# Optimization experiments

Measured on AMD Instinct MI355X. Metric: run time of the kernel, lower is better.

The kernel has to match this reference:

```python
import jax, jax.numpy as jnp
import numpy as np

D = 256  # subgraph_width
N_CLASSES = 10
EPS = 1e-5  # torch LayerNorm default


def _layernorm(x, g, b):
    mu = jnp.mean(x, axis=-1, keepdims=True)
    var = jnp.var(x, axis=-1, keepdims=True)
    return (x - mu) * jax.lax.rsqrt(var + EPS) * g + b


def setup_inputs() -> dict:
    key = jax.random.key(0)
    ks = jax.random.split(key, 16)
    B, T, N = 64, 512, 512
    traj = jax.random.normal(ks[0], (B, T, 2), dtype=jnp.float32)
    labels = jax.random.randint(ks[1], (B,), 0, N_CLASSES)
    h = jax.random.normal(ks[2], (B, N, D), dtype=jnp.float32)
    valid_len = jnp.maximum(jax.random.randint(ks[3], (B,), 0, N), 1)
    s = 0.02
    params = dict(
        emb=jax.random.normal(ks[4], (N_CLASSES, D), dtype=jnp.float32) * s,
        w_mlp=jax.random.normal(ks[5], (2, D), dtype=jnp.float32) * s,
        b_mlp=jnp.zeros((D,), jnp.float32),
        ln_g=jnp.ones((D,), jnp.float32),
        ln_b=jnp.zeros((D,), jnp.float32),
        wq=jax.random.normal(ks[6], (D, D), dtype=jnp.float32) * s,
        bq=jnp.zeros((D,), jnp.float32),
        wk=jax.random.normal(ks[7], (D, D), dtype=jnp.float32) * s,
        bk=jnp.zeros((D,), jnp.float32),
        wv=jax.random.normal(ks[8], (D, D), dtype=jnp.float32) * s,
        bv=jnp.zeros((D,), jnp.float32),
        w_out=jax.random.normal(ks[9], (D, 1), dtype=jnp.float32) * s,
        b_out=jnp.zeros((1,), jnp.float32),
    )
    return dict(traj=traj, labels=labels, h=h, valid_len=valid_len, **params)


def reference(traj, labels, h, valid_len, emb, w_mlp, b_mlp, ln_g, ln_b,
              wq, bq, wk, bk, wv, bv, w_out, b_out):
    # MLP(in=2, out=D, activation='leaky'): Linear -> LayerNorm -> LeakyReLU
    x = jax.nn.leaky_relu(_layernorm(traj @ w_mlp + b_mlp, ln_g, ln_b))  # [B,T,D]
    le = emb[labels]                          # [B,D]
    x = x + le[:, None, :]                    # embed-add
    # SelfAttentionWithKeyFCLayer: Q from x, K/V from h, scaled, key-masked by valid_len
    q = x @ wq + bq                            # [B,T,D]
    k = h @ wk + bk                            # [B,N,D]
    v = h @ wv + bv                            # [B,N,D]
    scores = jnp.einsum('btd,bnd->btn', q, k) / jnp.sqrt(jnp.float32(D))
    N = h.shape[1]
    key_mask = jnp.arange(N)[None, :] < valid_len[:, None]          # [B,N]
    scores = jnp.where(key_mask[:, None, :], scores, jnp.float32(-1e9))
    attn = jax.nn.softmax(scores, axis=-1)
    enc = jnp.einsum('btn,bnd->btd', attn, v)  # [B,T,D]
    pooled = jnp.max(enc, axis=1) + le          # [B,D]
    return jax.nn.sigmoid(pooled @ w_out + b_out)  # [B,1]
```

## Files before the change

### kernel.cpp

```cpp
#include <hip/hip_runtime.h>
#include <math.h>

typedef float f32x4 __attribute__((ext_vector_type(4)));
typedef __bf16 bf16x8 __attribute__((ext_vector_type(8)));
typedef unsigned short u16x8 __attribute__((ext_vector_type(8)));
typedef unsigned short u16x4 __attribute__((ext_vector_type(4)));
typedef unsigned int u32x4 __attribute__((ext_vector_type(4)));

#define MFMA(a, b, c) __builtin_amdgcn_mfma_f32_16x16x32_bf16((a), (b), (c), 0, 0, 0)

static __device__ __forceinline__ unsigned short f2bf(float f) {
  unsigned u = __float_as_uint(f);
  u += 0x7FFFu + ((u >> 16) & 1u);
  return (unsigned short)(u >> 16);
}
static __device__ __forceinline__ float bf2f(unsigned short s) {
  return __uint_as_float(((unsigned)s) << 16);
}
static __device__ __forceinline__ unsigned pack2bf(float lo, float hi) {
  return (unsigned)f2bf(lo) | ((unsigned)f2bf(hi) << 16);
}

static __device__ __forceinline__ int swz512(int row, int col) {
  return row * 512 + (col ^ ((((row & 7) ^ (col >> 6)) & 7) << 4));
}
static __device__ __forceinline__ int swzV(int d, int col) {
  return d * 64 + (col ^ (((d >> 1) & 3) << 4));
}
static __device__ __forceinline__ int swzO(int d, int col) {
  return d * 256 + (col ^ ((((d & 7) ^ (col >> 7)) & 7) << 4));
}

__global__ __launch_bounds__(256) void setup(
    const float* __restrict__ w0m, const float* __restrict__ w1m, const float* __restrict__ w2m,
    unsigned short* __restrict__ t0m, unsigned short* __restrict__ t1m, unsigned short* __restrict__ t2m,
    const float* __restrict__ w_mlp, const float* __restrict__ b_mlp, float* __restrict__ lnsc,
    const int* __restrict__ vlen, int* __restrict__ tasktab) {
  int bid = blockIdx.x;
  int t = threadIdx.x;
  if (bid == 48) {
    float w0 = w_mlp[t], w1 = w_mlp[256 + t], bb = b_mlp[t];
    float v[9] = {w0, w1, bb, w0 * w0, w1 * w1, w0 * w1, w0 * bb, w1 * bb, bb * bb};
    __shared__ float red[4][9];
#pragma unroll
    for (int j = 0; j < 9; ++j) {
      float s = v[j];
#pragma unroll
      for (int off = 32; off >= 1; off >>= 1) s += __shfl_xor(s, off, 64);
      v[j] = s;
    }
    if ((t & 63) == 0)
      for (int j = 0; j < 9; ++j) red[t >> 6][j] = v[j];
    __syncthreads();
    if (t < 9) lnsc[t] = red[0][t] + red[1][t] + red[2][t] + red[3][t];
    return;
  }
  if (bid == 49) {
    __shared__ int srank[64];
    if (t < 64) {
      int vb = vlen[t], r = 0;
      for (int j = 0; j < 64; ++j) {
        int vj = vlen[j];
        r += (vj > vb) || (vj == vb && j < t);
      }
      srank[r] = t;
    }
    __syncthreads();
    if (t < 64) {
      int r = t, b = srank[r];
      int xcd = r & 7, a = r >> 3;
      for (int tt = 0; tt < 4; ++tt)
        tasktab[(a * 4 + tt) * 8 + xcd] = (b << 2) | tt;
    }
    return;
  }
  int m = bid >> 4, t16 = bid & 15;
  const float* w = (m == 0) ? w0m : (m == 1) ? w1m : w2m;
  unsigned short* o = (m == 0) ? t0m : (m == 1) ? t1m : t2m;
  __shared__ float sm[64][65];
  int bi = t16 >> 2, bj = t16 & 3;
  for (int kb = 0; kb < 16; ++kb) {
    int idx = kb * 256 + t;
    int r = idx >> 6, c = idx & 63;
    sm[r][c] = w[(bi * 64 + r) * 256 + bj * 64 + c];
  }
  __syncthreads();
  for (int kb = 0; kb < 16; ++kb) {
    int idx = kb * 256 + t;
    int r = idx >> 6, c = idx & 63;
    int d = bj * 64 + r, e = bi * 64 + c;
    o[(e >> 5) * 8192 + d * 32 + (e & 31)] = f2bf(sm[c][r]);
  }
}

static __device__ __forceinline__ void gemm_direct(
    const unsigned short* __restrict__ Bpk, const unsigned short* Alds,
    int w, int g, int c15, f32x4 (&acc)[4][4]) {
  const unsigned short* bp = Bpk + (w * 64 + c15) * 32 + 8 * g;
#pragma unroll
  for (int c = 0; c < 8; ++c) {
    bf16x8 bfv[4];
#pragma unroll
    for (int nt = 0; nt < 4; ++nt)
      bfv[nt] = *(const bf16x8*)(bp + c * 8192 + nt * 512);
    bf16x8 af[4];
#pragma unroll
    for (int at = 0; at < 4; ++at)
      af[at] = *(const bf16x8*)((char*)Alds + swz512(at * 16 + c15, c * 64 + 16 * g));
    __builtin_amdgcn_s_setprio(1);
#pragma unroll
    for (int at = 0; at < 4; ++at)
#pragma unroll
      for (int nt = 0; nt < 4; ++nt) acc[at][nt] = MFMA(af[at], bfv[nt], acc[at][nt]);
    __builtin_amdgcn_s_setprio(0);
  }
}

__global__ __launch_bounds__(256, 4) void gemms(
    const float* __restrict__ traj, const int* __restrict__ labels, const float* __restrict__ emb,
    const float* __restrict__ w_mlp, const float* __restrict__ b_mlp,
    const float* __restrict__ ln_g, const float* __restrict__ ln_b,
    const float* __restrict__ lnsc, const unsigned short* __restrict__ wqPk,
    const float* __restrict__ bq, unsigned short* __restrict__ q,
    const float* __restrict__ h, const int* __restrict__ vlen,
    const unsigned short* __restrict__ wkPk, const float* __restrict__ bk,
    const unsigned short* __restrict__ wvPk, const float* __restrict__ bv,
    unsigned short* __restrict__ kout, unsigned short* __restrict__ vT) {
  __shared__ unsigned short Alds[64 * 256];
  int tid = threadIdx.x, w = tid >> 6, lane = tid & 63, g = lane >> 4, c15 = lane & 15;
  int bid = blockIdx.x;
  f32x4 acc[4][4];

  if (bid < 512) {
    int tile = bid, b = tile >> 3;
    {
      int rrow = tid >> 5, cb = (tid & 31) * 8;
      int lab = labels[b];
      f32x4 wa0 = *(const f32x4*)(w_mlp + cb), wa1 = *(const f32x4*)(w_mlp + cb + 4);
      f32x4 wb0 = *(const f32x4*)(w_mlp + 256 + cb), wb1 = *(const f32x4*)(w_mlp + 256 + cb + 4);
      f32x4 bm0 = *(const f32x4*)(b_mlp + cb), bm1 = *(const f32x4*)(b_mlp + cb + 4);
      f32x4 g0 = *(const f32x4*)(ln_g + cb), g1 = *(const f32x4*)(ln_g + cb + 4);
      f32x4 lb0 = *(const f32x4*)(ln_b + cb), lb1 = *(const f32x4*)(ln_b + cb + 4);
      f32x4 le0 = *(const f32x4*)(emb + lab * 256 + cb), le1 = *(const f32x4*)(emb + lab * 256 + cb + 4);
      float s0 = lnsc[0], s1 = lnsc[1], s2 = lnsc[2], s3 = lnsc[3], s4 = lnsc[4],
            s5 = lnsc[5], s6 = lnsc[6], s7 = lnsc[7], s8 = lnsc[8];
#pragma unroll
      for (int i = 0; i < 8; ++i) {
        int row = i * 8 + rrow, grow = tile * 64 + row;
        float t0 = traj[grow * 2], t1 = traj[grow * 2 + 1];
        float mu = (t0 * s0 + t1 * s1 + s2) * (1.f / 256.f);
        float ea2 = (t0 * t0 * s3 + t1 * t1 * s4 + s8 +
                     2.f * (t0 * t1 * s5 + t0 * s6 + t1 * s7)) * (1.f / 256.f);
        float rstd = rsqrtf(ea2 - mu * mu + 1e-5f);
        u16x8 pk;
#pragma unroll
        for (int j = 0; j < 4; ++j) {
          float a0 = t0 * wa0[j] + t1 * wb0[j] + bm0[j];
          float y0 = (a0 - mu) * rstd * g0[j] + lb0[j];
          pk[j] = f2bf((y0 > 0.f ? y0 : 0.01f * y0) + le0[j]);
          float a1 = t0 * wa1[j] + t1 * wb1[j] + bm1[j];
          float y1 = (a1 - mu) * rstd * g1[j] + lb1[j];
          pk[j + 4] = f2bf((y1 > 0.f ? y1 : 0.01f * y1) + le1[j]);
        }
        *(u16x8*)((char*)Alds + swz512(row, cb * 2)) = pk;
      }
    }
#pragma unroll
    for (int a = 0; a < 4; ++a)
#pragma unroll
      for (int n = 0; n < 4; ++n) acc[a][n] = (f32x4){0.f, 0.f, 0.f, 0.f};
    __syncthreads();
    gemm_direct(wqPk, Alds, w, g, c15, acc);
    __syncthreads();
#pragma unroll
    for (int at = 0; at < 4; ++at)
#pragma unroll
      for (int nt = 0; nt < 4; ++nt) {
        int col = w * 64 + nt * 16 + c15;
        float bb = bq[col];
#pragma unroll
        for (int r = 0; r < 4; ++r)
          *(unsigned short*)((char*)Alds + swz512(at * 16 + 4 * g + r, col * 2)) =
              f2bf(acc[at][nt][r] + bb);
      }
    __syncthreads();
    {
      int row = tid >> 2;
      for (int i = 0; i < 8; ++i) {
        int colb = (tid & 3) * 128 + i * 16;
        u16x8 vv = *(const u16x8*)((char*)Alds + swz512(row, colb));
        *(u16x8*)(q + (size_t)(tile * 64 + row) * 256 + colb / 2) = vv;
      }
    }
    return;
  }

  int tile = bid - 512;
  int b = tile >> 3;
  int nbase = (tile & 7) * 64;
  if (nbase >= vlen[b]) return;
  {
    const float* hb = h + (size_t)tile * 16384;
    f32x4 ha[8], hc[8];
#pragma unroll
    for (int i = 0; i < 8; ++i) {
      ha[i] = *(const f32x4*)(hb + i * 2048 + tid * 8);
      hc[i] = *(const f32x4*)(hb + i * 2048 + tid * 8 + 4);
    }
#pragma unroll
    for (int i = 0; i < 8; ++i) {
      u16x8 pk;
#pragma unroll
      for (int j = 0; j < 4; ++j) { pk[j] = f2bf(ha[i][j]); pk[j + 4] = f2bf(hc[i][j]); }
      *(u16x8*)((char*)Alds + swz512(i * 8 + (tid >> 5), (tid & 31) * 16)) = pk;
    }
  }
#pragma unroll
  for (int a = 0; a < 4; ++a)
#pragma unroll
    for (int n = 0; n < 4; ++n) acc[a][n] = (f32x4){0.f, 0.f, 0.f, 0.f};
  __syncthreads();

  gemm_direct(wvPk, Alds, w, g, c15, acc);
#pragma unroll
  for (int at = 0; at < 4; ++at)
#pragma unroll
    for (int nt = 0; nt < 4; ++nt) {
      int col = w * 64 + nt * 16 + c15;
      float bb = bv[col];
      u16x4 o;
#pragma unroll
      for (int r = 0; r < 4; ++r) o[r] = f2bf(acc[at][nt][r] + bb);
      *(u16x4*)(vT + (size_t)b * 131072 + (size_t)col * 512 + nbase + at * 16 + 4 * g) = o;
    }

#pragma unroll
  for (int a = 0; a < 4; ++a)
#pragma unroll
    for (int n = 0; n < 4; ++n) acc[a][n] = (f32x4){0.f, 0.f, 0.f, 0.f};
  gemm_direct(wkPk, Alds, w, g, c15, acc);
  __syncthreads();
#pragma unroll
  for (int at = 0; at < 4; ++at)
#pragma unroll
    for (int nt = 0; nt < 4; ++nt) {
      int col = w * 64 + nt * 16 + c15;
      float bb = bk[col];
#pragma unroll
      for (int r = 0; r < 4; ++r)
        *(unsigned short*)((char*)Alds + swz512(at * 16 + 4 * g + r, col * 2)) =
            f2bf(acc[at][nt][r] + bb);
    }
  __syncthreads();
  {
    int row = tid >> 2;
    for (int i = 0; i < 8; ++i) {
      int colb = (tid & 3) * 128 + i * 16;
      u16x8 vv = *(const u16x8*)((char*)Alds + swz512(row, colb));
      *(u16x8*)(kout + (size_t)(tile * 64 + row) * 256 + colb / 2) = vv;
    }
  }
}

__global__ __launch_bounds__(512) void attn(
    const unsigned short* __restrict__ q, const unsigned short* __restrict__ k,
    const unsigned short* __restrict__ vT, const int* __restrict__ valid_len,
    const int* __restrict__ tasktab, float* __restrict__ partial) {
  __shared__ unsigned short buf[2][16384];

  int task = tasktab[blockIdx.x];
  int b = task >> 2, tt = task & 3;
  int tid = threadIdx.x, w = tid >> 6, lane = tid & 63, g = lane >> 4, c15 = lane & 15;
  int vl = valid_len[b];
  int nit = (vl + 31) >> 5;

  bf16x8 qf[8];
  size_t qrow = (size_t)b * 512 + tt * 128 + w * 16 + c15;
#pragma unroll
  for (int kk = 0; kk < 8; ++kk)
    qf[kk] = *(const bf16x8*)(q + qrow * 256 + kk * 32 + 8 * g);

  f32x4 acco[16];
#pragma unroll
  for (int i = 0; i < 16; ++i) acco[i] = (f32x4){0.f, 0.f, 0.f, 0.f};
  float rs = 0.f;

  const unsigned short* kbase = k + (size_t)b * 512 * 256;
  const unsigned short* vbase = vT + (size_t)b * 131072;
  u16x8 kpre[2], vpre[2];

#pragma unroll
  for (int i = 0; i < 2; ++i) {
    int idx = tid + 512 * i, key = idx >> 5, s = idx & 31;
    kpre[i] = *(const u16x8*)(kbase + (size_t)key * 256 + s * 8);
  }
#pragma unroll
  for (int i = 0; i < 2; ++i) {
    int idx = tid + 512 * i, d = idx >> 2, s = idx & 3;
    vpre[i] = *(const u16x8*)(vbase + (size_t)d * 512 + s * 8);
  }
#pragma unroll
  for (int i = 0; i < 2; ++i) {
    int idx = tid + 512 * i, key = idx >> 5, s = idx & 31;
    *(u16x8*)((char*)buf[0] + swz512(key, s * 16)) = kpre[i];
  }
#pragma unroll
  for (int i = 0; i < 2; ++i) {
    int idx = tid + 512 * i, d = idx >> 2, s = idx & 3;
    *(u16x8*)((char*)(buf[0] + 8192) + swzV(d, s * 16)) = vpre[i];
  }

  for (int it = 0; it < nit; ++it) {
    int cur = it & 1;
    __syncthreads();
    bool pf = (it + 1 < nit);
    if (pf) {
      int n1 = (it + 1) * 32;
#pragma unroll
      for (int i = 0; i < 2; ++i) {
        int idx = tid + 512 * i, key = idx >> 5, s = idx & 31;
        kpre[i] = *(const u16x8*)(kbase + (size_t)(n1 + key) * 256 + s * 8);
      }
#pragma unroll
      for (int i = 0; i < 2; ++i) {
        int idx = tid + 512 * i, d = idx >> 2, s = idx & 3;
        vpre[i] = *(const u16x8*)(vbase + (size_t)d * 512 + n1 + s * 8);
      }
    }
    unsigned short* Klds = buf[cur];
    unsigned short* Vlds = buf[cur] + 8192;
    int n0 = it * 32;

    float p[2][4];
    unsigned u01[2], u23[2];
#pragma unroll
    for (int c = 0; c < 2; ++c) {
      f32x4 s4 = (f32x4){0.f, 0.f, 0.f, 0.f};
      __builtin_amdgcn_s_setprio(1);
#pragma unroll
      for (int kk = 0; kk < 8; ++kk) {
        bf16x8 kf = *(const bf16x8*)((char*)Klds + swz512(c * 16 + c15, kk * 64 + 16 * g));
        s4 = MFMA(kf, qf[kk], s4);
      }
      __builtin_amdgcn_s_setprio(0);
#pragma unroll
      for (int r = 0; r < 4; ++r) {
        int key = n0 + c * 16 + 4 * g + r;
        float pv = (key < vl) ? __expf(s4[r] * 0.0625f) : 0.f;
        p[c][r] = pv;
        rs += pv;
      }
      u01[c] = pack2bf(p[c][0], p[c][1]);
      u23[c] = pack2bf(p[c][2], p[c][3]);
    }
    int srcA = c15 | ((lane & 16) << 1);
    int srcB = srcA + 16;
    unsigned x0a = (unsigned)__shfl((int)u01[0], srcA, 64);
    unsigned x1a = (unsigned)__shfl((int)u01[1], srcA, 64);
    unsigned x0b = (unsigned)__shfl((int)u23[0], srcA, 64);
    unsigned x1b = (unsigned)__shfl((int)u23[1], srcA, 64);
    unsigned x0c = (unsigned)__shfl((int)u01[0], srcB, 64);
    unsigned x1c = (unsigned)__shfl((int)u01[1], srcB, 64);
    unsigned x0d = (unsigned)__shfl((int)u23[0], srcB, 64);
    unsigned x1d = (unsigned)__shfl((int)u23[1], srcB, 64);
    bool hi = g >= 2;
    union { u32x4 u; bf16x8 v; } pa;
    pa.u[0] = hi ? x1a : x0a;
    pa.u[1] = hi ? x1b : x0b;
    pa.u[2] = hi ? x1c : x0c;
    pa.u[3] = hi ? x1d : x0d;
    __builtin_amdgcn_s_setprio(1);
#pragma unroll
    for (int dt = 0; dt < 16; ++dt) {
      bf16x8 vf = *(const bf16x8*)((char*)Vlds + swzV(dt * 16 + c15, 16 * g));
      acco[dt] = MFMA(vf, pa.v, acco[dt]);
    }
    __builtin_amdgcn_s_setprio(0);
    if (pf) {
      unsigned short* Kn = buf[cur ^ 1];
      unsigned short* Vn = buf[cur ^ 1] + 8192;
#pragma unroll
      for (int i = 0; i < 2; ++i) {
        int idx = tid + 512 * i, key = idx >> 5, s = idx & 31;
        *(u16x8*)((char*)Kn + swz512(key, s * 16)) = kpre[i];
      }
#pragma unroll
      for (int i = 0; i < 2; ++i) {
        int idx = tid + 512 * i, d = idx >> 2, s = idx & 3;
        *(u16x8*)((char*)Vn + swzV(d, s * 16)) = vpre[i];
      }
    }
  }
  rs += __shfl_xor(rs, 16, 64);
  rs += __shfl_xor(rs, 32, 64);
  float inv = 1.f / rs;
  __syncthreads();
  int qcol = w * 16 + c15;
#pragma unroll
  for (int dt = 0; dt < 16; ++dt)
#pragma unroll
    for (int r = 0; r < 4; ++r) {
      int d = dt * 16 + 4 * g + r;
      *(unsigned short*)((char*)buf + swzO(d, qcol * 2)) = f2bf(acco[dt][r] * inv);
    }
  __syncthreads();
  {
    int d = tid & 255, half = tid >> 8;
    float m = -1e30f;
    for (int i = 0; i < 8; ++i) {
      u16x8 vv = *(const u16x8*)((char*)buf + swzO(d, half * 128 + i * 16));
#pragma unroll
      for (int j = 0; j < 8; ++j) m = fmaxf(m, bf2f(vv[j]));
    }
    partial[(((size_t)b * 4 + tt) * 2 + half) * 256 + d] = m;
  }
}

__global__ __launch_bounds__(256) void finalize(
    const float* __restrict__ partial, const float* __restrict__ emb,
    const int* __restrict__ labels, const float* __restrict__ w_out,
    const float* __restrict__ b_out, float* __restrict__ out) {
  int b = blockIdx.x, t = threadIdx.x;
  float m = -1e30f;
#pragma unroll
  for (int s8 = 0; s8 < 8; ++s8)
    m = fmaxf(m, partial[((size_t)b * 8 + s8) * 256 + t]);
  m += emb[labels[b] * 256 + t];
  __shared__ float red[256];
  red[t] = m * w_out[t];
  __syncthreads();
  for (int s = 128; s > 0; s >>= 1) {
    if (t < s) red[t] += red[t + s];
    __syncthreads();
  }
  if (t == 0) out[b] = 1.f / (1.f + __expf(-(red[0] + b_out[0])));
}

extern "C" void kernel_launch(void* const* d_in, const int* in_sizes, int n_in,
                              void* d_out, int out_size, void* d_ws, size_t ws_size,
                              hipStream_t stream) {
  const float* traj   = (const float*)d_in[0];
  const int*   labels = (const int*)d_in[1];
  const float* h      = (const float*)d_in[2];
  const int*   vlen   = (const int*)d_in[3];
  const float* emb    = (const float*)d_in[4];
  const float* w_mlp  = (const float*)d_in[5];
  const float* b_mlp  = (const float*)d_in[6];
  const float* ln_g   = (const float*)d_in[7];
  const float* ln_b   = (const float*)d_in[8];
  const float* wq     = (const float*)d_in[9];
  const float* bq     = (const float*)d_in[10];
  const float* wk     = (const float*)d_in[11];
  const float* bk     = (const float*)d_in[12];
  const float* wv     = (const float*)d_in[13];
  const float* bv     = (const float*)d_in[14];
  const float* w_out  = (const float*)d_in[15];
  const float* b_out  = (const float*)d_in[16];
  float* out = (float*)d_out;

  unsigned short* qb   = (unsigned short*)d_ws;
  unsigned short* kb   = qb + (size_t)32768 * 256;
  unsigned short* vT   = kb + (size_t)32768 * 256;
  unsigned short* wqPk = vT + (size_t)32768 * 256;
  unsigned short* wkPk = wqPk + 65536;
  unsigned short* wvPk = wkPk + 65536;
  float* lnsc    = (float*)(wvPk + 65536);
  float* partial = lnsc + 16;
  int*   tasktab = (int*)(partial + 64 * 8 * 256);

  setup<<<50, 256, 0, stream>>>(wq, wk, wv, wqPk, wkPk, wvPk, w_mlp, b_mlp, lnsc,
                                vlen, tasktab);
  gemms<<<1024, 256, 0, stream>>>(traj, labels, emb, w_mlp, b_mlp, ln_g, ln_b,
                                  lnsc, wqPk, bq, qb, h, vlen, wkPk, bk, wvPk, bv,
                                  kb, vT);
  attn<<<256, 512, 0, stream>>>(qb, kb, vT, vlen, tasktab, partial);
  finalize<<<64, 256, 0, stream>>>(partial, emb, labels, w_out, b_out, out);
}
```

Before: 76.83 us.

## Fuse MLP/LayerNorm and Q projection into attention kernel, 2 query tiles per wave

The embedding MLP, LayerNorm and Q GEMM move out of the gemms kernel and into the attention kernel. Each attention block computes its 128 query rows in LDS and keeps them in registers, so the bf16 Q round trip through global memory goes away and the gemms launch shrinks to the K/V blocks only. The attention block drops from 512 to 256 threads, and each wave now handles two 16-row query tiles. Each K/V fragment loaded from LDS is therefore reused for twice as many MFMAs. The trade-off is much higher register pressure (launch_bounds 1) and fewer waves per block for latency hiding, with the Q GEMM now serialized ahead of the attention loop.

```diff
diff --git a/kernel.cpp b/kernel.cpp
--- a/kernel.cpp
+++ b/kernel.cpp
@@ -117,88 +117,17 @@
 }
 
 __global__ __launch_bounds__(256, 4) void gemms(
-    const float* __restrict__ traj, const int* __restrict__ labels, const float* __restrict__ emb,
-    const float* __restrict__ w_mlp, const float* __restrict__ b_mlp,
-    const float* __restrict__ ln_g, const float* __restrict__ ln_b,
-    const float* __restrict__ lnsc, const unsigned short* __restrict__ wqPk,
-    const float* __restrict__ bq, unsigned short* __restrict__ q,
     const float* __restrict__ h, const int* __restrict__ vlen,
     const unsigned short* __restrict__ wkPk, const float* __restrict__ bk,
     const unsigned short* __restrict__ wvPk, const float* __restrict__ bv,
     unsigned short* __restrict__ kout, unsigned short* __restrict__ vT) {
   __shared__ unsigned short Alds[64 * 256];
   int tid = threadIdx.x, w = tid >> 6, lane = tid & 63, g = lane >> 4, c15 = lane & 15;
-  int bid = blockIdx.x;
-  f32x4 acc[4][4];
-
-  if (bid < 512) {
-    int tile = bid, b = tile >> 3;
-    {
-      int rrow = tid >> 5, cb = (tid & 31) * 8;
-      int lab = labels[b];
-      f32x4 wa0 = *(const f32x4*)(w_mlp + cb), wa1 = *(const f32x4*)(w_mlp + cb + 4);
-      f32x4 wb0 = *(const f32x4*)(w_mlp + 256 + cb), wb1 = *(const f32x4*)(w_mlp + 256 + cb + 4);
-      f32x4 bm0 = *(const f32x4*)(b_mlp + cb), bm1 = *(const f32x4*)(b_mlp + cb + 4);
-      f32x4 g0 = *(const f32x4*)(ln_g + cb), g1 = *(const f32x4*)(ln_g + cb + 4);
-      f32x4 lb0 = *(const f32x4*)(ln_b + cb), lb1 = *(const f32x4*)(ln_b + cb + 4);
-      f32x4 le0 = *(const f32x4*)(emb + lab * 256 + cb), le1 = *(const f32x4*)(emb + lab * 256 + cb + 4);
-      float s0 = lnsc[0], s1 = lnsc[1], s2 = lnsc[2], s3 = lnsc[3], s4 = lnsc[4],
-            s5 = lnsc[5], s6 = lnsc[6], s7 = lnsc[7], s8 = lnsc[8];
-#pragma unroll
-      for (int i = 0; i < 8; ++i) {
-        int row = i * 8 + rrow, grow = tile * 64 + row;
-        float t0 = traj[grow * 2], t1 = traj[grow * 2 + 1];
-        float mu = (t0 * s0 + t1 * s1 + s2) * (1.f / 256.f);
-        float ea2 = (t0 * t0 * s3 + t1 * t1 * s4 + s8 +
-                     2.f * (t0 * t1 * s5 + t0 * s6 + t1 * s7)) * (1.f / 256.f);
-        float rstd = rsqrtf(ea2 - mu * mu + 1e-5f);
-        u16x8 pk;
-#pragma unroll
-        for (int j = 0; j < 4; ++j) {
-          float a0 = t0 * wa0[j] + t1 * wb0[j] + bm0[j];
-          float y0 = (a0 - mu) * rstd * g0[j] + lb0[j];
-          pk[j] = f2bf((y0 > 0.f ? y0 : 0.01f * y0) + le0[j]);
-          float a1 = t0 * wa1[j] + t1 * wb1[j] + bm1[j];
-          float y1 = (a1 - mu) * rstd * g1[j] + lb1[j];
-          pk[j + 4] = f2bf((y1 > 0.f ? y1 : 0.01f * y1) + le1[j]);
-        }
-        *(u16x8*)((char*)Alds + swz512(row, cb * 2)) = pk;
-      }
-    }
-#pragma unroll
-    for (int a = 0; a < 4; ++a)
-#pragma unroll
-      for (int n = 0; n < 4; ++n) acc[a][n] = (f32x4){0.f, 0.f, 0.f, 0.f};
-    __syncthreads();
-    gemm_direct(wqPk, Alds, w, g, c15, acc);
-    __syncthreads();
-#pragma unroll
-    for (int at = 0; at < 4; ++at)
-#pragma unroll
-      for (int nt = 0; nt < 4; ++nt) {
-        int col = w * 64 + nt * 16 + c15;
-        float bb = bq[col];
-#pragma unroll
-        for (int r = 0; r < 4; ++r)
-          *(unsigned short*)((char*)Alds + swz512(at * 16 + 4 * g + r, col * 2)) =
-              f2bf(acc[at][nt][r] + bb);
-      }
-    __syncthreads();
-    {
-      int row = tid >> 2;
-      for (int i = 0; i < 8; ++i) {
-        int colb = (tid & 3) * 128 + i * 16;
-        u16x8 vv = *(const u16x8*)((char*)Alds + swz512(row, colb));
-        *(u16x8*)(q + (size_t)(tile * 64 + row) * 256 + colb / 2) = vv;
-      }
-    }
-    return;
-  }
-
-  int tile = bid - 512;
+  int tile = blockIdx.x;
   int b = tile >> 3;
   int nbase = (tile & 7) * 64;
   if (nbase >= vlen[b]) return;
+  f32x4 acc[4][4];
   {
     const float* hb = h + (size_t)tile * 16384;
     f32x4 ha[8], hc[8];
@@ -262,10 +191,15 @@
   }
 }
 
-__global__ __launch_bounds__(512) void attn(
-    const unsigned short* __restrict__ q, const unsigned short* __restrict__ k,
-    const unsigned short* __restrict__ vT, const int* __restrict__ valid_len,
-    const int* __restrict__ tasktab, float* __restrict__ partial) {
+__global__ __launch_bounds__(256, 1) void attn(
+    const float* __restrict__ traj, const int* __restrict__ labels,
+    const float* __restrict__ emb, const float* __restrict__ w_mlp,
+    const float* __restrict__ b_mlp, const float* __restrict__ ln_g,
+    const float* __restrict__ ln_b, const float* __restrict__ lnsc,
+    const unsigned short* __restrict__ wqPk, const float* __restrict__ bq,
+    const unsigned short* __restrict__ k, const unsigned short* __restrict__ vT,
+    const int* __restrict__ valid_len, const int* __restrict__ tasktab,
+    float* __restrict__ partial) {
   __shared__ unsigned short buf[2][16384];
 
   int task = tasktab[blockIdx.x];
@@ -274,39 +208,115 @@
   int vl = valid_len[b];
   int nit = (vl + 31) >> 5;
 
-  bf16x8 qf[8];
-  size_t qrow = (size_t)b * 512 + tt * 128 + w * 16 + c15;
-#pragma unroll
-  for (int kk = 0; kk < 8; ++kk)
-    qf[kk] = *(const bf16x8*)(q + qrow * 256 + kk * 32 + 8 * g);
-
-  f32x4 acco[16];
-#pragma unroll
-  for (int i = 0; i < 16; ++i) acco[i] = (f32x4){0.f, 0.f, 0.f, 0.f};
-  float rs = 0.f;
+  {
+    int rrow = tid >> 5, cb = (tid & 31) * 8;
+    int lab = labels[b];
+    f32x4 wa0 = *(const f32x4*)(w_mlp + cb), wa1 = *(const f32x4*)(w_mlp + cb + 4);
+    f32x4 wb0 = *(const f32x4*)(w_mlp + 256 + cb), wb1 = *(const f32x4*)(w_mlp + 256 + cb + 4);
+    f32x4 bm0 = *(const f32x4*)(b_mlp + cb), bm1 = *(const f32x4*)(b_mlp + cb + 4);
+    f32x4 g0 = *(const f32x4*)(ln_g + cb), g1 = *(const f32x4*)(ln_g + cb + 4);
+    f32x4 lb0 = *(const f32x4*)(ln_b + cb), lb1 = *(const f32x4*)(ln_b + cb + 4);
+    f32x4 le0 = *(const f32x4*)(emb + lab * 256 + cb), le1 = *(const f32x4*)(emb + lab * 256 + cb + 4);
+    float s0 = lnsc[0], s1 = lnsc[1], s2 = lnsc[2], s3 = lnsc[3], s4 = lnsc[4],
+          s5 = lnsc[5], s6 = lnsc[6], s7 = lnsc[7], s8 = lnsc[8];
+#pragma unroll
+    for (int i = 0; i < 16; ++i) {
+      int row = i * 8 + rrow, grow = b * 512 + tt * 128 + row;
+      float t0 = traj[grow * 2], t1 = traj[grow * 2 + 1];
+      float mu = (t0 * s0 + t1 * s1 + s2) * (1.f / 256.f);
+      float ea2 = (t0 * t0 * s3 + t1 * t1 * s4 + s8 +
+                   2.f * (t0 * t1 * s5 + t0 * s6 + t1 * s7)) * (1.f / 256.f);
+      float rstd = rsqrtf(ea2 - mu * mu + 1e-5f);
+      u16x8 pk;
+#pragma unroll
+      for (int j = 0; j < 4; ++j) {
+        float a0 = t0 * wa0[j] + t1 * wb0[j] + bm0[j];
+        float y0 = (a0 - mu) * rstd * g0[j] + lb0[j];
+        pk[j] = f2bf((y0 > 0.f ? y0 : 0.01f * y0) + le0[j]);
+        float a1 = t0 * wa1[j] + t1 * wb1[j] + bm1[j];
+        float y1 = (a1 - mu) * rstd * g1[j] + lb1[j];
+        pk[j + 4] = f2bf((y1 > 0.f ? y1 : 0.01f * y1) + le1[j]);
+      }
+      *(u16x8*)((char*)buf + swz512(row, cb * 2)) = pk;
+    }
+  }
+  __syncthreads();
+
+  f32x4 qacc[8][4];
+#pragma unroll
+  for (int a = 0; a < 8; ++a)
+#pragma unroll
+    for (int n = 0; n < 4; ++n) qacc[a][n] = (f32x4){0.f, 0.f, 0.f, 0.f};
+  {
+    const unsigned short* bp = wqPk + (w * 64 + c15) * 32 + 8 * g;
+#pragma unroll
+    for (int c = 0; c < 8; ++c) {
+      bf16x8 bfv[4];
+#pragma unroll
+      for (int nt = 0; nt < 4; ++nt)
+        bfv[nt] = *(const bf16x8*)(bp + c * 8192 + nt * 512);
+      bf16x8 af[8];
+#pragma unroll
+      for (int at = 0; at < 8; ++at)
+        af[at] = *(const bf16x8*)((char*)buf + swz512(at * 16 + c15, c * 64 + 16 * g));
+      __builtin_amdgcn_s_setprio(1);
+#pragma unroll
+      for (int at = 0; at < 8; ++at)
+#pragma unroll
+        for (int nt = 0; nt < 4; ++nt) qacc[at][nt] = MFMA(af[at], bfv[nt], qacc[at][nt]);
+      __builtin_amdgcn_s_setprio(0);
+    }
+  }
+  __syncthreads();
+#pragma unroll
+  for (int nt = 0; nt < 4; ++nt) {
+    int col = w * 64 + nt * 16 + c15;
+    float bb = bq[col];
+#pragma unroll
+    for (int at = 0; at < 8; ++at)
+#pragma unroll
+      for (int r = 0; r < 4; ++r)
+        *(unsigned short*)((char*)buf + swz512(at * 16 + 4 * g + r, col * 2)) =
+            f2bf(qacc[at][nt][r] + bb);
+  }
+  __syncthreads();
+  bf16x8 qf[2][8];
+#pragma unroll
+  for (int qt = 0; qt < 2; ++qt)
+#pragma unroll
+    for (int kk = 0; kk < 8; ++kk)
+      qf[qt][kk] = *(const bf16x8*)((char*)buf + swz512(qt * 64 + w * 16 + c15, kk * 64 + 16 * g));
+  __syncthreads();
+
+  f32x4 acco[2][16];
+#pragma unroll
+  for (int qt = 0; qt < 2; ++qt)
+#pragma unroll
+    for (int i = 0; i < 16; ++i) acco[qt][i] = (f32x4){0.f, 0.f, 0.f, 0.f};
+  float rs[2] = {0.f, 0.f};
 
   const unsigned short* kbase = k + (size_t)b * 512 * 256;
   const unsigned short* vbase = vT + (size_t)b * 131072;
-  u16x8 kpre[2], vpre[2];
-
-#pragma unroll
-  for (int i = 0; i < 2; ++i) {
-    int idx = tid + 512 * i, key = idx >> 5, s = idx & 31;
+  u16x8 kpre[4], vpre[4];
+
+#pragma unroll
+  for (int i = 0; i < 4; ++i) {
+    int idx = tid + 256 * i, key = idx >> 5, s = idx & 31;
     kpre[i] = *(const u16x8*)(kbase + (size_t)key * 256 + s * 8);
   }
 #pragma unroll
-  for (int i = 0; i < 2; ++i) {
-    int idx = tid + 512 * i, d = idx >> 2, s = idx & 3;
+  for (int i = 0; i < 4; ++i) {
+    int idx = tid + 256 * i, d = idx >> 2, s = idx & 3;
     vpre[i] = *(const u16x8*)(vbase + (size_t)d * 512 + s * 8);
   }
 #pragma unroll
-  for (int i = 0; i < 2; ++i) {
-    int idx = tid + 512 * i, key = idx >> 5, s = idx & 31;
+  for (int i = 0; i < 4; ++i) {
+    int idx = tid + 256 * i, key = idx >> 5, s = idx & 31;
     *(u16x8*)((char*)buf[0] + swz512(key, s * 16)) = kpre[i];
   }
 #pragma unroll
-  for (int i = 0; i < 2; ++i) {
-    int idx = tid + 512 * i, d = idx >> 2, s = idx & 3;
+  for (int i = 0; i < 4; ++i) {
+    int idx = tid + 256 * i, d = idx >> 2, s = idx & 3;
     *(u16x8*)((char*)(buf[0] + 8192) + swzV(d, s * 16)) = vpre[i];
   }
 
@@ -317,13 +327,13 @@
     if (pf) {
       int n1 = (it + 1) * 32;
 #pragma unroll
-      for (int i = 0; i < 2; ++i) {
-        int idx = tid + 512 * i, key = idx >> 5, s = idx & 31;
+      for (int i = 0; i < 4; ++i) {
+        int idx = tid + 256 * i, key = idx >> 5, s = idx & 31;
         kpre[i] = *(const u16x8*)(kbase + (size_t)(n1 + key) * 256 + s * 8);
       }
 #pragma unroll
-      for (int i = 0; i < 2; ++i) {
-        int idx = tid + 512 * i, d = idx >> 2, s = idx & 3;
+      for (int i = 0; i < 4; ++i) {
+        int idx = tid + 256 * i, d = idx >> 2, s = idx & 3;
         vpre[i] = *(const u16x8*)(vbase + (size_t)d * 512 + n1 + s * 8);
       }
     }
@@ -331,88 +341,108 @@
     unsigned short* Vlds = buf[cur] + 8192;
     int n0 = it * 32;
 
-    float p[2][4];
-    unsigned u01[2], u23[2];
-#pragma unroll
-    for (int c = 0; c < 2; ++c) {
-      f32x4 s4 = (f32x4){0.f, 0.f, 0.f, 0.f};
-      __builtin_amdgcn_s_setprio(1);
+    f32x4 s4[2][2];
+#pragma unroll
+    for (int qt = 0; qt < 2; ++qt)
+#pragma unroll
+      for (int c = 0; c < 2; ++c) s4[qt][c] = (f32x4){0.f, 0.f, 0.f, 0.f};
+    __builtin_amdgcn_s_setprio(1);
+#pragma unroll
+    for (int c = 0; c < 2; ++c)
 #pragma unroll
       for (int kk = 0; kk < 8; ++kk) {
         bf16x8 kf = *(const bf16x8*)((char*)Klds + swz512(c * 16 + c15, kk * 64 + 16 * g));
-        s4 = MFMA(kf, qf[kk], s4);
-      }
-      __builtin_amdgcn_s_setprio(0);
-#pragma unroll
-      for (int r = 0; r < 4; ++r) {
-        int key = n0 + c * 16 + 4 * g + r;
-        float pv = (key < vl) ? __expf(s4[r] * 0.0625f) : 0.f;
-        p[c][r] = pv;
-        rs += pv;
-      }
-      u01[c] = pack2bf(p[c][0], p[c][1]);
-      u23[c] = pack2bf(p[c][2], p[c][3]);
-    }
+        s4[0][c] = MFMA(kf, qf[0][kk], s4[0][c]);
+        s4[1][c] = MFMA(kf, qf[1][kk], s4[1][c]);
+      }
+    __builtin_amdgcn_s_setprio(0);
+    unsigned u01[2][2], u23[2][2];
+#pragma unroll
+    for (int qt = 0; qt < 2; ++qt)
+#pragma unroll
+      for (int c = 0; c < 2; ++c) {
+        float p4[4];
+#pragma unroll
+        for (int r = 0; r < 4; ++r) {
+          int key = n0 + c * 16 + 4 * g + r;
+          float pv = (key < vl) ? __expf(s4[qt][c][r] * 0.0625f) : 0.f;
+          p4[r] = pv;
+          rs[qt] += pv;
+        }
+        u01[qt][c] = pack2bf(p4[0], p4[1]);
+        u23[qt][c] = pack2bf(p4[2], p4[3]);
+      }
     int srcA = c15 | ((lane & 16) << 1);
     int srcB = srcA + 16;
-    unsigned x0a = (unsigned)__shfl((int)u01[0], srcA, 64);
-    unsigned x1a = (unsigned)__shfl((int)u01[1], srcA, 64);
-    unsigned x0b = (unsigned)__shfl((int)u23[0], srcA, 64);
-    unsigned x1b = (unsigned)__shfl((int)u23[1], srcA, 64);
-    unsigned x0c = (unsigned)__shfl((int)u01[0], srcB, 64);
-    unsigned x1c = (unsigned)__shfl((int)u01[1], srcB, 64);
-    unsigned x0d = (unsigned)__shfl((int)u23[0], srcB, 64);
-    unsigned x1d = (unsigned)__shfl((int)u23[1], srcB, 64);
     bool hi = g >= 2;
-    union { u32x4 u; bf16x8 v; } pa;
-    pa.u[0] = hi ? x1a : x0a;
-    pa.u[1] = hi ? x1b : x0b;
-    pa.u[2] = hi ? x1c : x0c;
-    pa.u[3] = hi ? x1d : x0d;
+    union { u32x4 u; bf16x8 v; } pa[2];
+#pragma unroll
+    for (int qt = 0; qt < 2; ++qt) {
+      unsigned x0a = (unsigned)__shfl((int)u01[qt][0], srcA, 64);
+      unsigned x1a = (unsigned)__shfl((int)u01[qt][1], srcA, 64);
+      unsigned x0b = (unsigned)__shfl((int)u23[qt][0], srcA, 64);
+      unsigned x1b = (unsigned)__shfl((int)u23[qt][1], srcA, 64);
+      unsigned x0c = (unsigned)__shfl((int)u01[qt][0], srcB, 64);
+      unsigned x1c = (unsigned)__shfl((int)u01[qt][1], srcB, 64);
+      unsigned x0d = (unsigned)__shfl((int)u23[qt][0], srcB, 64);
+      unsigned x1d = (unsigned)__shfl((int)u23[qt][1], srcB, 64);
+      pa[qt].u[0] = hi ? x1a : x0a;
+      pa[qt].u[1] = hi ? x1b : x0b;
+      pa[qt].u[2] = hi ? x1c : x0c;
+      pa[qt].u[3] = hi ? x1d : x0d;
+    }
     __builtin_amdgcn_s_setprio(1);
 #pragma unroll
     for (int dt = 0; dt < 16; ++dt) {
       bf16x8 vf = *(const bf16x8*)((char*)Vlds + swzV(dt * 16 + c15, 16 * g));
-      acco[dt] = MFMA(vf, pa.v, acco[dt]);
+      acco[0][dt] = MFMA(vf, pa[0].v, acco[0][dt]);
+      acco[1][dt] = MFMA(vf, pa[1].v, acco[1][dt]);
     }
     __builtin_amdgcn_s_setprio(0);
     if (pf) {
       unsigned short* Kn = buf[cur ^ 1];
       unsigned short* Vn = buf[cur ^ 1] + 8192;
 #pragma unroll
-      for (int i = 0; i < 2; ++i) {
-        int idx = tid + 512 * i, key = idx >> 5, s = idx & 31;
+      for (int i = 0; i < 4; ++i) {
+        int idx = tid + 256 * i, key = idx >> 5, s = idx & 31;
         *(u16x8*)((char*)Kn + swz512(key, s * 16)) = kpre[i];
       }
 #pragma unroll
-      for (int i = 0; i < 2; ++i) {
-        int idx = tid + 512 * i, d = idx >> 2, s = idx & 3;
+      for (int i = 0; i < 4; ++i) {
+        int idx = tid + 256 * i, d = idx >> 2, s = idx & 3;
         *(u16x8*)((char*)Vn + swzV(d, s * 16)) = vpre[i];
       }
     }
   }
-  rs += __shfl_xor(rs, 16, 64);
-  rs += __shfl_xor(rs, 32, 64);
-  float inv = 1.f / rs;
-  __syncthreads();
-  int qcol = w * 16 + c15;
-#pragma unroll
-  for (int dt = 0; dt < 16; ++dt)
-#pragma unroll
-    for (int r = 0; r < 4; ++r) {
-      int d = dt * 16 + 4 * g + r;
-      *(unsigned short*)((char*)buf + swzO(d, qcol * 2)) = f2bf(acco[dt][r] * inv);
-    }
+  float inv[2];
+#pragma unroll
+  for (int qt = 0; qt < 2; ++qt) {
+    rs[qt] += __shfl_xor(rs[qt], 16, 64);
+    rs[qt] += __shfl_xor(rs[qt], 32, 64);
+    inv[qt] = 1.f / rs[qt];
+  }
+  __syncthreads();
+#pragma unroll
+  for (int qt = 0; qt < 2; ++qt) {
+    int qcol = qt * 64 + w * 16 + c15;
+#pragma unroll
+    for (int dt = 0; dt < 16; ++dt)
+#pragma unroll
+      for (int r = 0; r < 4; ++r) {
+        int d = dt * 16 + 4 * g + r;
+        *(unsigned short*)((char*)buf + swzO(d, qcol * 2)) = f2bf(acco[qt][dt][r] * inv[qt]);
+      }
+  }
   __syncthreads();
   {
-    int d = tid & 255, half = tid >> 8;
+    int d = tid;
     float m = -1e30f;
-    for (int i = 0; i < 8; ++i) {
-      u16x8 vv = *(const u16x8*)((char*)buf + swzO(d, half * 128 + i * 16));
+    for (int i = 0; i < 16; ++i) {
+      u16x8 vv = *(const u16x8*)((char*)buf + swzO(d, i * 16));
 #pragma unroll
       for (int j = 0; j < 8; ++j) m = fmaxf(m, bf2f(vv[j]));
     }
-    partial[(((size_t)b * 4 + tt) * 2 + half) * 256 + d] = m;
+    partial[((size_t)b * 4 + tt) * 256 + d] = m;
   }
 }
 
@@ -423,8 +453,8 @@
   int b = blockIdx.x, t = threadIdx.x;
   float m = -1e30f;
 #pragma unroll
-  for (int s8 = 0; s8 < 8; ++s8)
-    m = fmaxf(m, partial[((size_t)b * 8 + s8) * 256 + t]);
+  for (int s4 = 0; s4 < 4; ++s4)
+    m = fmaxf(m, partial[((size_t)b * 4 + s4) * 256 + t]);
   m += emb[labels[b] * 256 + t];
   __shared__ float red[256];
   red[t] = m * w_out[t];
@@ -458,21 +488,19 @@
   const float* b_out  = (const float*)d_in[16];
   float* out = (float*)d_out;
 
-  unsigned short* qb   = (unsigned short*)d_ws;
-  unsigned short* kb   = qb + (size_t)32768 * 256;
+  unsigned short* kb   = (unsigned short*)d_ws;
   unsigned short* vT   = kb + (size_t)32768 * 256;
   unsigned short* wqPk = vT + (size_t)32768 * 256;
   unsigned short* wkPk = wqPk + 65536;
   unsigned short* wvPk = wkPk + 65536;
   float* lnsc    = (float*)(wvPk + 65536);
   float* partial = lnsc + 16;
-  int*   tasktab = (int*)(partial + 64 * 8 * 256);
+  int*   tasktab = (int*)(partial + 64 * 4 * 256);
 
   setup<<<50, 256, 0, stream>>>(wq, wk, wv, wqPk, wkPk, wvPk, w_mlp, b_mlp, lnsc,
                                 vlen, tasktab);
-  gemms<<<1024, 256, 0, stream>>>(traj, labels, emb, w_mlp, b_mlp, ln_g, ln_b,
-                                  lnsc, wqPk, bq, qb, h, vlen, wkPk, bk, wvPk, bv,
-                                  kb, vT);
-  attn<<<256, 512, 0, stream>>>(qb, kb, vT, vlen, tasktab, partial);
+  gemms<<<512, 256, 0, stream>>>(h, vlen, wkPk, bk, wvPk, bv, kb, vT);
+  attn<<<256, 256, 0, stream>>>(traj, labels, emb, w_mlp, b_mlp, ln_g, ln_b, lnsc,
+                                wqPk, bq, kb, vT, vlen, tasktab, partial);
   finalize<<<64, 256, 0, stream>>>(partial, emb, labels, w_out, b_out, out);
 }
```

Measured after the change: 86.46 us. +12.5%, slower.

## Fuse Q projection into attention kernel and split K/V GEMMs across waves

Applied to the files above, without the earlier changes.

The MLP+LayerNorm+embedding prologue and the Q projection move from the gemms kernel into the attention kernel. Each attention block now computes its own 128 rows of Q in LDS and reads them straight into registers, so Q is never written to or read back from global memory. The gemms kernel becomes K/V only, launched with 512-thread blocks where four waves compute V and four compute K concurrently, using a separate LDS buffer for K. The cost is extra prologue work and synchronisation inside the attention kernel, plus higher register and LDS pressure there.

```diff
diff --git a/kernel.cpp b/kernel.cpp
--- a/kernel.cpp
+++ b/kernel.cpp
@@ -116,103 +116,33 @@
   }
 }
 
-__global__ __launch_bounds__(256, 4) void gemms(
-    const float* __restrict__ traj, const int* __restrict__ labels, const float* __restrict__ emb,
-    const float* __restrict__ w_mlp, const float* __restrict__ b_mlp,
-    const float* __restrict__ ln_g, const float* __restrict__ ln_b,
-    const float* __restrict__ lnsc, const unsigned short* __restrict__ wqPk,
-    const float* __restrict__ bq, unsigned short* __restrict__ q,
+__global__ __launch_bounds__(512, 4) void gemms(
     const float* __restrict__ h, const int* __restrict__ vlen,
     const unsigned short* __restrict__ wkPk, const float* __restrict__ bk,
     const unsigned short* __restrict__ wvPk, const float* __restrict__ bv,
     unsigned short* __restrict__ kout, unsigned short* __restrict__ vT) {
   __shared__ unsigned short Alds[64 * 256];
+  __shared__ unsigned short Klds[64 * 256];
   int tid = threadIdx.x, w = tid >> 6, lane = tid & 63, g = lane >> 4, c15 = lane & 15;
-  int bid = blockIdx.x;
-  f32x4 acc[4][4];
-
-  if (bid < 512) {
-    int tile = bid, b = tile >> 3;
-    {
-      int rrow = tid >> 5, cb = (tid & 31) * 8;
-      int lab = labels[b];
-      f32x4 wa0 = *(const f32x4*)(w_mlp + cb), wa1 = *(const f32x4*)(w_mlp + cb + 4);
-      f32x4 wb0 = *(const f32x4*)(w_mlp + 256 + cb), wb1 = *(const f32x4*)(w_mlp + 256 + cb + 4);
-      f32x4 bm0 = *(const f32x4*)(b_mlp + cb), bm1 = *(const f32x4*)(b_mlp + cb + 4);
-      f32x4 g0 = *(const f32x4*)(ln_g + cb), g1 = *(const f32x4*)(ln_g + cb + 4);
-      f32x4 lb0 = *(const f32x4*)(ln_b + cb), lb1 = *(const f32x4*)(ln_b + cb + 4);
-      f32x4 le0 = *(const f32x4*)(emb + lab * 256 + cb), le1 = *(const f32x4*)(emb + lab * 256 + cb + 4);
-      float s0 = lnsc[0], s1 = lnsc[1], s2 = lnsc[2], s3 = lnsc[3], s4 = lnsc[4],
-            s5 = lnsc[5], s6 = lnsc[6], s7 = lnsc[7], s8 = lnsc[8];
-#pragma unroll
-      for (int i = 0; i < 8; ++i) {
-        int row = i * 8 + rrow, grow = tile * 64 + row;
-        float t0 = traj[grow * 2], t1 = traj[grow * 2 + 1];
-        float mu = (t0 * s0 + t1 * s1 + s2) * (1.f / 256.f);
-        float ea2 = (t0 * t0 * s3 + t1 * t1 * s4 + s8 +
-                     2.f * (t0 * t1 * s5 + t0 * s6 + t1 * s7)) * (1.f / 256.f);
-        float rstd = rsqrtf(ea2 - mu * mu + 1e-5f);
-        u16x8 pk;
-#pragma unroll
-        for (int j = 0; j < 4; ++j) {
-          float a0 = t0 * wa0[j] + t1 * wb0[j] + bm0[j];
-          float y0 = (a0 - mu) * rstd * g0[j] + lb0[j];
-          pk[j] = f2bf((y0 > 0.f ? y0 : 0.01f * y0) + le0[j]);
-          float a1 = t0 * wa1[j] + t1 * wb1[j] + bm1[j];
-          float y1 = (a1 - mu) * rstd * g1[j] + lb1[j];
-          pk[j + 4] = f2bf((y1 > 0.f ? y1 : 0.01f * y1) + le1[j]);
-        }
-        *(u16x8*)((char*)Alds + swz512(row, cb * 2)) = pk;
-      }
-    }
-#pragma unroll
-    for (int a = 0; a < 4; ++a)
-#pragma unroll
-      for (int n = 0; n < 4; ++n) acc[a][n] = (f32x4){0.f, 0.f, 0.f, 0.f};
-    __syncthreads();
-    gemm_direct(wqPk, Alds, w, g, c15, acc);
-    __syncthreads();
-#pragma unroll
-    for (int at = 0; at < 4; ++at)
-#pragma unroll
-      for (int nt = 0; nt < 4; ++nt) {
-        int col = w * 64 + nt * 16 + c15;
-        float bb = bq[col];
-#pragma unroll
-        for (int r = 0; r < 4; ++r)
-          *(unsigned short*)((char*)Alds + swz512(at * 16 + 4 * g + r, col * 2)) =
-              f2bf(acc[at][nt][r] + bb);
-      }
-    __syncthreads();
-    {
-      int row = tid >> 2;
-      for (int i = 0; i < 8; ++i) {
-        int colb = (tid & 3) * 128 + i * 16;
-        u16x8 vv = *(const u16x8*)((char*)Alds + swz512(row, colb));
-        *(u16x8*)(q + (size_t)(tile * 64 + row) * 256 + colb / 2) = vv;
-      }
-    }
-    return;
-  }
-
-  int tile = bid - 512;
+  int tile = blockIdx.x;
   int b = tile >> 3;
   int nbase = (tile & 7) * 64;
   if (nbase >= vlen[b]) return;
+  f32x4 acc[4][4];
   {
     const float* hb = h + (size_t)tile * 16384;
-    f32x4 ha[8], hc[8];
-#pragma unroll
-    for (int i = 0; i < 8; ++i) {
-      ha[i] = *(const f32x4*)(hb + i * 2048 + tid * 8);
-      hc[i] = *(const f32x4*)(hb + i * 2048 + tid * 8 + 4);
-    }
-#pragma unroll
-    for (int i = 0; i < 8; ++i) {
+    f32x4 ha[4], hc[4];
+#pragma unroll
+    for (int i = 0; i < 4; ++i) {
+      ha[i] = *(const f32x4*)(hb + i * 4096 + tid * 8);
+      hc[i] = *(const f32x4*)(hb + i * 4096 + tid * 8 + 4);
+    }
+#pragma unroll
+    for (int i = 0; i < 4; ++i) {
       u16x8 pk;
 #pragma unroll
       for (int j = 0; j < 4; ++j) { pk[j] = f2bf(ha[i][j]); pk[j + 4] = f2bf(hc[i][j]); }
-      *(u16x8*)((char*)Alds + swz512(i * 8 + (tid >> 5), (tid & 31) * 16)) = pk;
+      *(u16x8*)((char*)Alds + swz512(i * 16 + (tid >> 5), (tid & 31) * 16)) = pk;
     }
   }
 #pragma unroll
@@ -221,51 +151,54 @@
     for (int n = 0; n < 4; ++n) acc[a][n] = (f32x4){0.f, 0.f, 0.f, 0.f};
   __syncthreads();
 
-  gemm_direct(wvPk, Alds, w, g, c15, acc);
-#pragma unroll
-  for (int at = 0; at < 4; ++at)
-#pragma unroll
-    for (int nt = 0; nt < 4; ++nt) {
-      int col = w * 64 + nt * 16 + c15;
-      float bb = bv[col];
-      u16x4 o;
-#pragma unroll
-      for (int r = 0; r < 4; ++r) o[r] = f2bf(acc[at][nt][r] + bb);
-      *(u16x4*)(vT + (size_t)b * 131072 + (size_t)col * 512 + nbase + at * 16 + 4 * g) = o;
-    }
-
-#pragma unroll
-  for (int a = 0; a < 4; ++a)
-#pragma unroll
-    for (int n = 0; n < 4; ++n) acc[a][n] = (f32x4){0.f, 0.f, 0.f, 0.f};
-  gemm_direct(wkPk, Alds, w, g, c15, acc);
-  __syncthreads();
-#pragma unroll
-  for (int at = 0; at < 4; ++at)
-#pragma unroll
-    for (int nt = 0; nt < 4; ++nt) {
-      int col = w * 64 + nt * 16 + c15;
-      float bb = bk[col];
-#pragma unroll
-      for (int r = 0; r < 4; ++r)
-        *(unsigned short*)((char*)Alds + swz512(at * 16 + 4 * g + r, col * 2)) =
-            f2bf(acc[at][nt][r] + bb);
-    }
-  __syncthreads();
-  {
+  int w4 = w & 3;
+  if (w < 4) {
+    gemm_direct(wvPk, Alds, w4, g, c15, acc);
+#pragma unroll
+    for (int at = 0; at < 4; ++at)
+#pragma unroll
+      for (int nt = 0; nt < 4; ++nt) {
+        int col = w4 * 64 + nt * 16 + c15;
+        float bb = bv[col];
+        u16x4 o;
+#pragma unroll
+        for (int r = 0; r < 4; ++r) o[r] = f2bf(acc[at][nt][r] + bb);
+        *(u16x4*)(vT + (size_t)b * 131072 + (size_t)col * 512 + nbase + at * 16 + 4 * g) = o;
+      }
+  } else {
+    gemm_direct(wkPk, Alds, w4, g, c15, acc);
+#pragma unroll
+    for (int at = 0; at < 4; ++at)
+#pragma unroll
+      for (int nt = 0; nt < 4; ++nt) {
+        int col = w4 * 64 + nt * 16 + c15;
+        float bb = bk[col];
+#pragma unroll
+        for (int r = 0; r < 4; ++r)
+          *(unsigned short*)((char*)Klds + swz512(at * 16 + 4 * g + r, col * 2)) =
+              f2bf(acc[at][nt][r] + bb);
+      }
+  }
+  __syncthreads();
+  if (tid < 256) {
     int row = tid >> 2;
     for (int i = 0; i < 8; ++i) {
       int colb = (tid & 3) * 128 + i * 16;
-      u16x8 vv = *(const u16x8*)((char*)Alds + swz512(row, colb));
+      u16x8 vv = *(const u16x8*)((char*)Klds + swz512(row, colb));
       *(u16x8*)(kout + (size_t)(tile * 64 + row) * 256 + colb / 2) = vv;
     }
   }
 }
 
-__global__ __launch_bounds__(512) void attn(
-    const unsigned short* __restrict__ q, const unsigned short* __restrict__ k,
-    const unsigned short* __restrict__ vT, const int* __restrict__ valid_len,
-    const int* __restrict__ tasktab, float* __restrict__ partial) {
+__global__ __launch_bounds__(512, 2) void attn(
+    const float* __restrict__ traj, const int* __restrict__ labels,
+    const float* __restrict__ emb, const float* __restrict__ w_mlp,
+    const float* __restrict__ b_mlp, const float* __restrict__ ln_g,
+    const float* __restrict__ ln_b, const float* __restrict__ lnsc,
+    const unsigned short* __restrict__ wqPk, const float* __restrict__ bq,
+    const unsigned short* __restrict__ k, const unsigned short* __restrict__ vT,
+    const int* __restrict__ valid_len, const int* __restrict__ tasktab,
+    float* __restrict__ partial) {
   __shared__ unsigned short buf[2][16384];
 
   int task = tasktab[blockIdx.x];
@@ -273,12 +206,86 @@
   int tid = threadIdx.x, w = tid >> 6, lane = tid & 63, g = lane >> 4, c15 = lane & 15;
   int vl = valid_len[b];
   int nit = (vl + 31) >> 5;
-
+  int wq4 = w & 3;
+
+  {
+    int rrow = tid >> 5, cb = (tid & 31) * 8;
+    int lab = labels[b];
+    f32x4 wa0 = *(const f32x4*)(w_mlp + cb), wa1 = *(const f32x4*)(w_mlp + cb + 4);
+    f32x4 wb0 = *(const f32x4*)(w_mlp + 256 + cb), wb1 = *(const f32x4*)(w_mlp + 256 + cb + 4);
+    f32x4 bm0 = *(const f32x4*)(b_mlp + cb), bm1 = *(const f32x4*)(b_mlp + cb + 4);
+    f32x4 g0 = *(const f32x4*)(ln_g + cb), g1 = *(const f32x4*)(ln_g + cb + 4);
+    f32x4 lb0 = *(const f32x4*)(ln_b + cb), lb1 = *(const f32x4*)(ln_b + cb + 4);
+    f32x4 le0 = *(const f32x4*)(emb + lab * 256 + cb), le1 = *(const f32x4*)(emb + lab * 256 + cb + 4);
+    float s0 = lnsc[0], s1 = lnsc[1], s2 = lnsc[2], s3 = lnsc[3], s4_ = lnsc[4],
+          s5 = lnsc[5], s6 = lnsc[6], s7 = lnsc[7], s8 = lnsc[8];
+#pragma unroll
+    for (int i = 0; i < 8; ++i) {
+      int row = i * 16 + rrow, grow = b * 512 + tt * 128 + row;
+      float t0 = traj[grow * 2], t1 = traj[grow * 2 + 1];
+      float mu = (t0 * s0 + t1 * s1 + s2) * (1.f / 256.f);
+      float ea2 = (t0 * t0 * s3 + t1 * t1 * s4_ + s8 +
+                   2.f * (t0 * t1 * s5 + t0 * s6 + t1 * s7)) * (1.f / 256.f);
+      float rstd = rsqrtf(ea2 - mu * mu + 1e-5f);
+      u16x8 pk;
+#pragma unroll
+      for (int j = 0; j < 4; ++j) {
+        float a0 = t0 * wa0[j] + t1 * wb0[j] + bm0[j];
+        float y0 = (a0 - mu) * rstd * g0[j] + lb0[j];
+        pk[j] = f2bf((y0 > 0.f ? y0 : 0.01f * y0) + le0[j]);
+        float a1 = t0 * wa1[j] + t1 * wb1[j] + bm1[j];
+        float y1 = (a1 - mu) * rstd * g1[j] + lb1[j];
+        pk[j + 4] = f2bf((y1 > 0.f ? y1 : 0.01f * y1) + le1[j]);
+      }
+      *(u16x8*)((char*)buf + swz512(row, cb * 2)) = pk;
+    }
+  }
+  __syncthreads();
+
+  {
+    f32x4 qacc[4][4];
+#pragma unroll
+    for (int a = 0; a < 4; ++a)
+#pragma unroll
+      for (int n = 0; n < 4; ++n) qacc[a][n] = (f32x4){0.f, 0.f, 0.f, 0.f};
+    int rbase = (w >> 2) * 64;
+    const unsigned short* bp = wqPk + (wq4 * 64 + c15) * 32 + 8 * g;
+#pragma unroll
+    for (int c = 0; c < 8; ++c) {
+      bf16x8 bfv[4];
+#pragma unroll
+      for (int nt = 0; nt < 4; ++nt)
+        bfv[nt] = *(const bf16x8*)(bp + c * 8192 + nt * 512);
+      bf16x8 af[4];
+#pragma unroll
+      for (int at = 0; at < 4; ++at)
+        af[at] = *(const bf16x8*)((char*)buf + swz512(rbase + at * 16 + c15, c * 64 + 16 * g));
+      __builtin_amdgcn_s_setprio(1);
+#pragma unroll
+      for (int at = 0; at < 4; ++at)
+#pragma unroll
+        for (int nt = 0; nt < 4; ++nt) qacc[at][nt] = MFMA(af[at], bfv[nt], qacc[at][nt]);
+      __builtin_amdgcn_s_setprio(0);
+    }
+    __syncthreads();
+#pragma unroll
+    for (int nt = 0; nt < 4; ++nt) {
+      int col = wq4 * 64 + nt * 16 + c15;
+      float bb = bq[col];
+#pragma unroll
+      for (int at = 0; at < 4; ++at)
+#pragma unroll
+        for (int r = 0; r < 4; ++r)
+          *(unsigned short*)((char*)buf + swz512(rbase + at * 16 + 4 * g + r, col * 2)) =
+              f2bf(qacc[at][nt][r] + bb);
+    }
+  }
+  __syncthreads();
   bf16x8 qf[8];
-  size_t qrow = (size_t)b * 512 + tt * 128 + w * 16 + c15;
 #pragma unroll
   for (int kk = 0; kk < 8; ++kk)
-    qf[kk] = *(const bf16x8*)(q + qrow * 256 + kk * 32 + 8 * g);
+    qf[kk] = *(const bf16x8*)((char*)buf + swz512(w * 16 + c15, kk * 64 + 16 * g));
+  __syncthreads();
 
   f32x4 acco[16];
 #pragma unroll
@@ -458,8 +465,7 @@
   const float* b_out  = (const float*)d_in[16];
   float* out = (float*)d_out;
 
-  unsigned short* qb   = (unsigned short*)d_ws;
-  unsigned short* kb   = qb + (size_t)32768 * 256;
+  unsigned short* kb   = (unsigned short*)d_ws;
   unsigned short* vT   = kb + (size_t)32768 * 256;
   unsigned short* wqPk = vT + (size_t)32768 * 256;
   unsigned short* wkPk = wqPk + 65536;
@@ -470,9 +476,8 @@
 
   setup<<<50, 256, 0, stream>>>(wq, wk, wv, wqPk, wkPk, wvPk, w_mlp, b_mlp, lnsc,
                                 vlen, tasktab);
-  gemms<<<1024, 256, 0, stream>>>(traj, labels, emb, w_mlp, b_mlp, ln_g, ln_b,
-                                  lnsc, wqPk, bq, qb, h, vlen, wkPk, bk, wvPk, bv,
-                                  kb, vT);
-  attn<<<256, 512, 0, stream>>>(qb, kb, vT, vlen, tasktab, partial);
+  gemms<<<512, 512, 0, stream>>>(h, vlen, wkPk, bk, wvPk, bv, kb, vT);
+  attn<<<256, 512, 0, stream>>>(traj, labels, emb, w_mlp, b_mlp, ln_g, ln_b, lnsc,
+                                wqPk, bq, kb, vT, vlen, tasktab, partial);
   finalize<<<64, 256, 0, stream>>>(partial, emb, labels, w_out, b_out, out);
 }
```

Result: faster. 72.88 us (-5.1%).
